# Optimization experiments

Measured on AMD Instinct MI355X. Metric: run time of the kernel, lower is better.

The kernel has to match this reference:

```python
import jax, jax.numpy as jnp
import numpy as np

D = 1024
H = 16
HD = D // H
EPS = 1e-5


def layer_norm(x, g, b):
    mu = jnp.mean(x, axis=-1, keepdims=True)
    var = jnp.var(x, axis=-1, keepdims=True)
    return (x - mu) * jax.lax.rsqrt(var + EPS) * g + b


def setup_inputs() -> dict:
    key = jax.random.key(0)
    ks = jax.random.split(key, 16)
    s = 0.02
    return {
        "x": jax.random.normal(ks[0], (2, 2048, D), jnp.float32),
        "ln1_g": jnp.ones((D,), jnp.float32),
        "ln1_b": jnp.zeros((D,), jnp.float32),
        "Wq": jax.random.normal(ks[1], (D, D), jnp.float32) * s,
        "bq": jnp.zeros((D,), jnp.float32),
        "Wk": jax.random.normal(ks[2], (D, D), jnp.float32) * s,
        "bk": jnp.zeros((D,), jnp.float32),
        "Wv": jax.random.normal(ks[3], (D, D), jnp.float32) * s,
        "bv": jnp.zeros((D,), jnp.float32),
        "Wo": jax.random.normal(ks[4], (D, D), jnp.float32) * s,
        "bo": jnp.zeros((D,), jnp.float32),
        "ln2_g": jnp.ones((D,), jnp.float32),
        "ln2_b": jnp.zeros((D,), jnp.float32),
        "W1": jax.random.normal(ks[5], (D, 4 * D), jnp.float32) * s,
        "b1": jnp.zeros((4 * D,), jnp.float32),
        "W2": jax.random.normal(ks[6], (4 * D, D), jnp.float32) * s,
        "b2": jnp.zeros((D,), jnp.float32),
    }


def reference(x, ln1_g, ln1_b, Wq, bq, Wk, bk, Wv, bv, Wo, bo, ln2_g, ln2_b, W1, b1, W2, b2):
    B, T, _ = x.shape
    # --- attention sub-block (pre-LN) ---
    h = layer_norm(x, ln1_g, ln1_b)
    q = (h @ Wq + bq).reshape(B, T, H, HD).transpose(0, 2, 1, 3)  # [B,H,T,hd]
    k = (h @ Wk + bk).reshape(B, T, H, HD).transpose(0, 2, 1, 3)
    v = (h @ Wv + bv).reshape(B, T, H, HD).transpose(0, 2, 1, 3)
    scores = jnp.einsum("bhqd,bhkd->bhqk", q, k)  # full O(T^2) scores as in source
    causal = jnp.tril(jnp.ones((T, T), bool))
    scores = jnp.where(causal, scores, -jnp.inf)
    w = jax.nn.softmax(scores / np.sqrt(HD), axis=-1)
    ctx = jnp.einsum("bhqk,bhkd->bhqd", w, v)
    ctx = ctx.transpose(0, 2, 1, 3).reshape(B, T, D)
    x = x + (ctx @ Wo + bo)
    # --- MLP sub-block (pre-LN) ---
    h = layer_norm(x, ln2_g, ln2_b)
    h = jax.nn.gelu(h @ W1 + b1, approximate=False)
    x = x + (h @ W2 + b2)
    return x
```

## Files before the change

kernel.cpp:

```cpp
#include <hip/hip_runtime.h>
#include <math.h>


typedef _Float16 half8 __attribute__((ext_vector_type(8)));
typedef _Float16 half4v __attribute__((ext_vector_type(4)));
typedef float floatx4 __attribute__((ext_vector_type(4)));

#define DMODEL 1024
#define SEQT   2048
#define NTOK   4096
#define NHEAD  16
#define HDIM   64

__device__ __forceinline__ void llds16(const _Float16* g, _Float16* l) {
  __builtin_amdgcn_global_load_lds(
      (const __attribute__((address_space(1))) void*)g,
      (__attribute__((address_space(3))) void*)l, 16, 0, 0);
}

__global__ __launch_bounds__(256) void wtrans_kernel(
    const float* __restrict__ Wq, const float* __restrict__ Wk,
    const float* __restrict__ Wv, const float* __restrict__ Wo,
    const float* __restrict__ W1, const float* __restrict__ W2,
    _Float16* __restrict__ wt_base) {
  __shared__ float tilebuf[32][33];
  int id = blockIdx.x;
  const float* src; _Float16* dst; int K, N, t;
  if (id < 4096) {
    int s = id >> 10;
    src = (s == 0) ? Wq : (s == 1) ? Wk : (s == 2) ? Wv : Wo;
    dst = wt_base + (size_t)s * (1024 * 1024);
    K = 1024; N = 1024; t = id & 1023;
  } else if (id < 8192) {
    src = W1; dst = wt_base + (size_t)4 * 1024 * 1024; K = 1024; N = 4096; t = id - 4096;
  } else {
    src = W2; dst = wt_base + (size_t)8 * 1024 * 1024; K = 4096; N = 1024; t = id - 8192;
  }
  int tilesN = N >> 5;
  int tk = t / tilesN, tn = t % tilesN;
  int c = threadIdx.x & 31, r0 = threadIdx.x >> 5;
#pragma unroll
  for (int i = 0; i < 4; ++i) {
    int r = r0 + i * 8;
    tilebuf[r][c] = src[(size_t)(tk * 32 + r) * N + tn * 32 + c];
  }
  __syncthreads();
#pragma unroll
  for (int i = 0; i < 4; ++i) {
    int r = r0 + i * 8;
    dst[(size_t)(tn * 32 + r) * K + tk * 32 + c] = (_Float16)tilebuf[c][r];
  }
}

__global__ __launch_bounds__(256) void ln_kernel(
    const float* __restrict__ x, const float* __restrict__ g,
    const float* __restrict__ b, _Float16* __restrict__ out) {
  int row = blockIdx.x;
  int t = threadIdx.x;
  const float4 xv = ((const float4*)(x + (size_t)row * DMODEL))[t];
  float s = xv.x + xv.y + xv.z + xv.w;
  float s2 = xv.x * xv.x + xv.y * xv.y + xv.z * xv.z + xv.w * xv.w;
#pragma unroll
  for (int off = 32; off; off >>= 1) {
    s += __shfl_down(s, off);
    s2 += __shfl_down(s2, off);
  }
  __shared__ float red[8];
  int wid = t >> 6;
  if ((t & 63) == 0) { red[wid] = s; red[wid + 4] = s2; }
  __syncthreads();
  s = red[0] + red[1] + red[2] + red[3];
  s2 = red[4] + red[5] + red[6] + red[7];
  float mu = s * (1.0f / DMODEL);
  float var = s2 * (1.0f / DMODEL) - mu * mu;
  float rstd = rsqrtf(var + 1e-5f);
  const float4 gv = ((const float4*)g)[t];
  const float4 bv = ((const float4*)b)[t];
  half4v o;
  o[0] = (_Float16)((xv.x - mu) * rstd * gv.x + bv.x);
  o[1] = (_Float16)((xv.y - mu) * rstd * gv.y + bv.y);
  o[2] = (_Float16)((xv.z - mu) * rstd * gv.z + bv.z);
  o[3] = (_Float16)((xv.w - mu) * rstd * gv.w + bv.w);
  *(half4v*)(out + (size_t)row * DMODEL + t * 4) = o;
}

template <int MODE>
__global__ __launch_bounds__(256) void gemm_kernel(
    const _Float16* __restrict__ A, const _Float16* __restrict__ Bt0, int K,
    const float* __restrict__ bias0, const float* __restrict__ bias1,
    const float* __restrict__ bias2, const float* __restrict__ res,
    float* __restrict__ outf, _Float16* __restrict__ outh) {
  constexpr int NT = (MODE == 1) ? 64 : 128;
  constexpr int MI = (NT == 128) ? 4 : 2;
  constexpr int BCH = NT / 64;
  __shared__ __align__(16) _Float16 As[2][128 * 32];
  __shared__ __align__(16) _Float16 Bs[2][NT * 32];
  const int tid = threadIdx.x;
  const int m0 = blockIdx.x * 128;
  const _Float16* Bt;
  const float* bias;
  _Float16* outh_sel = outh;
  int n0, sel = 0;
  if (MODE == 0) {
    sel = blockIdx.y >> 3;
    n0 = (blockIdx.y & 7) * 128;
    Bt = Bt0 + (size_t)sel * (1024 * 1024);
    bias = (sel == 0) ? bias0 : (sel == 1) ? bias1 : bias2;
    outh_sel = outh + (size_t)sel * ((size_t)NTOK * DMODEL);
  } else {
    n0 = blockIdx.y * NT;
    Bt = Bt0;
    bias = bias0;
  }
  const int w = tid >> 6, lane = tid & 63;
  const int l15 = lane & 15, q8 = lane >> 4;
  const int wrow = (NT == 128) ? (w >> 1) * 64 : w * 32;
  const int wcol = (NT == 128) ? (w & 1) * 64 : 0;

  const _Float16* gA[2]; int ldsA[2];
  const _Float16* gB[BCH]; int ldsB[BCH];
#pragma unroll
  for (int i = 0; i < 2; ++i) {
    int c0 = i * 256 + w * 64;
    int idx = c0 + lane;
    int m = idx >> 2, kq = (idx & 3) * 8;
    gA[i] = A + (size_t)(m0 + m) * K + kq;
    ldsA[i] = c0 * 8;
  }
#pragma unroll
  for (int i = 0; i < BCH; ++i) {
    int c0 = i * 256 + w * 64;
    int idx = c0 + lane;
    int m = idx >> 2, kq = (idx & 3) * 8;
    gB[i] = Bt + (size_t)(n0 + m) * K + kq;
    ldsB[i] = c0 * 8;
  }

  auto stage = [&](int buf) {
#pragma unroll
    for (int i = 0; i < 2; ++i) {
      llds16(gA[i], &As[buf][ldsA[i]]);
      gA[i] += 32;
    }
#pragma unroll
    for (int i = 0; i < BCH; ++i) {
      llds16(gB[i], &Bs[buf][ldsB[i]]);
      gB[i] += 32;
    }
  };

  floatx4 acc[MI][4];
#pragma unroll
  for (int i = 0; i < MI; ++i)
#pragma unroll
    for (int j = 0; j < 4; ++j) acc[i][j] = (floatx4){0.f, 0.f, 0.f, 0.f};

  const int nk = K >> 5;
  stage(0);
  __syncthreads();
  for (int t = 0; t < nk; ++t) {
    const int buf = t & 1;
    if (t + 1 < nk) stage(buf ^ 1);
    half8 af[MI], bf[4];
#pragma unroll
    for (int i = 0; i < MI; ++i)
      af[i] = *(const half8*)&As[buf][(wrow + i * 16 + l15) * 32 + q8 * 8];
#pragma unroll
    for (int j = 0; j < 4; ++j)
      bf[j] = *(const half8*)&Bs[buf][(wcol + j * 16 + l15) * 32 + q8 * 8];
#pragma unroll
    for (int i = 0; i < MI; ++i)
#pragma unroll
      for (int j = 0; j < 4; ++j)
        acc[i][j] = __builtin_amdgcn_mfma_f32_16x16x32_f16(af[i], bf[j], acc[i][j], 0, 0, 0);
    __syncthreads();
  }

#pragma unroll
  for (int i = 0; i < MI; ++i) {
    int rowb = m0 + wrow + i * 16 + q8 * 4;
#pragma unroll
    for (int j = 0; j < 4; ++j) {
      int col = n0 + wcol + j * 16 + l15;
      float bval = bias[col];
#pragma unroll
      for (int r = 0; r < 4; ++r) {
        int row = rowb + r;
        float v = acc[i][j][r] + bval;
        if (MODE == 0) {
          int bb = row >> 11, tt = row & 2047;
          int hh = col >> 6, hd = col & 63;
          if (sel == 2)
            outh_sel[((size_t)(bb * NHEAD + hh) * HDIM + hd) * SEQT + tt] = (_Float16)v;
          else
            outh_sel[((size_t)(bb * NHEAD + hh) * SEQT + tt) * HDIM + hd] = (_Float16)v;
        } else if (MODE == 1) {
          v += res[(size_t)row * 1024 + col];
          outf[(size_t)row * 1024 + col] = v;
        } else {
          float z = 1.5957691216f * v * (1.0f + 0.044715f * v * v);
          float gl = v / (1.0f + __expf(-z));
          outh[(size_t)row * 4096 + col] = (_Float16)gl;
        }
      }
    }
  }
}

__global__ __launch_bounds__(256) void attn_kernel(
    const _Float16* __restrict__ q, const _Float16* __restrict__ k,
    const _Float16* __restrict__ vt, _Float16* __restrict__ ctx) {
  __shared__ __align__(16) _Float16 Ks[2][64 * 64];
  __shared__ __align__(16) _Float16 Vs[2][64 * 64];
  __shared__ __align__(16) _Float16 Ps[64 * 72];
  __shared__ float Lpart[4][64];
  const int tid = threadIdx.x;
  const int w = tid >> 6, lane = tid & 63;
  const int l15 = lane & 15, q8 = lane >> 4;
  const int bh = blockIdx.y;
  const int pr = blockIdx.x;
  const size_t base = (size_t)bh * SEQT * HDIM;

  const _Float16* gk0[2]; const _Float16* gv0[2]; int ldsc[2];
#pragma unroll
  for (int i = 0; i < 2; ++i) {
    int c = i * 256 + w * 64 + lane;
    int r = c >> 3, gc = ((c & 7) ^ (r & 7)) * 8;
    gk0[i] = k + base + (size_t)r * HDIM + gc;
    gv0[i] = vt + base + (size_t)r * SEQT + gc;
    ldsc[i] = c * 8;
  }
  auto stage = [&](int kt, int buf) {
#pragma unroll
    for (int i = 0; i < 2; ++i) {
      llds16(gk0[i] + (size_t)kt * (64 * HDIM), &Ks[buf][ldsc[i]]);
      llds16(gv0[i] + kt * 64, &Vs[buf][ldsc[i]]);
    }
  };

  const int rswA = (l15 & 7);
  const int cs0 = (q8 ^ rswA) * 8;
  const int cs1 = ((4 + q8) ^ rswA) * 8;

  int s = 0;
  stage(0, 0);
  __syncthreads();
  for (int ph = 0; ph < 2; ++ph) {
    const int qtile = ph ? 31 - pr : pr;
    const int ntile = qtile + 1;
    half8 bq[4][2];
#pragma unroll
    for (int nt = 0; nt < 4; ++nt) {
      const half8* qp = (const half8*)(q + base + (size_t)(qtile * 64 + nt * 16 + l15) * HDIM);
      bq[nt][0] = qp[q8];
      bq[nt][1] = qp[4 + q8];
    }
    floatx4 acc[4];
#pragma unroll
    for (int j = 0; j < 4; ++j) acc[j] = (floatx4){0.f, 0.f, 0.f, 0.f};
    float lsum[4] = {0.f, 0.f, 0.f, 0.f};

    for (int jt = 0; jt < ntile; ++jt, ++s) {
      const int buf = s & 1;
      if (s + 1 < 33) {
        int sn = s + 1;
        int nkt = (sn <= pr) ? sn : sn - (pr + 1);
        stage(nkt, buf ^ 1);
      }
      half8 ak0 = *(const half8*)&Ks[buf][(w * 16 + l15) * 64 + cs0];
      half8 ak1 = *(const half8*)&Ks[buf][(w * 16 + l15) * 64 + cs1];
      floatx4 sv[4];
#pragma unroll
      for (int nt = 0; nt < 4; ++nt) {
        sv[nt] = __builtin_amdgcn_mfma_f32_16x16x32_f16(ak0, bq[nt][0],
                                                        (floatx4){0.f, 0.f, 0.f, 0.f}, 0, 0, 0);
        sv[nt] = __builtin_amdgcn_mfma_f32_16x16x32_f16(ak1, bq[nt][1], sv[nt], 0, 0, 0);
      }
      const bool diag = (jt == ntile - 1);
#pragma unroll
      for (int nt = 0; nt < 4; ++nt) {
        half4v phv;
#pragma unroll
        for (int r = 0; r < 4; ++r) {
          float p = __expf(sv[nt][r] * 0.125f);
          if (diag) {
            p = (w * 16 + q8 * 4 + r <= nt * 16 + l15) ? p : 0.f;
          }
          lsum[nt] += p;
          phv[r] = (_Float16)p;
        }
        *(half4v*)&Ps[(nt * 16 + l15) * 72 + w * 16 + q8 * 4] = phv;
      }
      __syncthreads();
      half8 ap0 = *(const half8*)&Ps[(w * 16 + l15) * 72 + q8 * 8];
      half8 ap1 = *(const half8*)&Ps[(w * 16 + l15) * 72 + 32 + q8 * 8];
#pragma unroll
      for (int ntd = 0; ntd < 4; ++ntd) {
        half8 bv0 = *(const half8*)&Vs[buf][(ntd * 16 + l15) * 64 + cs0];
        half8 bv1 = *(const half8*)&Vs[buf][(ntd * 16 + l15) * 64 + cs1];
        acc[ntd] = __builtin_amdgcn_mfma_f32_16x16x32_f16(ap0, bv0, acc[ntd], 0, 0, 0);
        acc[ntd] = __builtin_amdgcn_mfma_f32_16x16x32_f16(ap1, bv1, acc[ntd], 0, 0, 0);
      }
      __syncthreads();
    }

#pragma unroll
    for (int nt = 0; nt < 4; ++nt) {
      lsum[nt] += __shfl_xor(lsum[nt], 16);
      lsum[nt] += __shfl_xor(lsum[nt], 32);
      if (q8 == 0) Lpart[w][nt * 16 + l15] = lsum[nt];
    }
    __syncthreads();
    const int b = bh >> 4, h = bh & 15;
#pragma unroll
    for (int r = 0; r < 4; ++r) {
      int qr = w * 16 + q8 * 4 + r;
      float inv = 1.0f / (Lpart[0][qr] + Lpart[1][qr] + Lpart[2][qr] + Lpart[3][qr]);
      int tg = qtile * 64 + qr;
      _Float16* op = ctx + ((size_t)(b * SEQT + tg)) * DMODEL + h * HDIM;
#pragma unroll
      for (int ntd = 0; ntd < 4; ++ntd)
        op[ntd * 16 + l15] = (_Float16)(acc[ntd][r] * inv);
    }
  }
}

extern "C" void kernel_launch(void* const* d_in, const int* in_sizes, int n_in,
                              void* d_out, int out_size, void* d_ws, size_t ws_size,
                              hipStream_t stream) {
  (void)in_sizes; (void)n_in; (void)out_size; (void)ws_size;
  const float* x    = (const float*)d_in[0];
  const float* ln1g = (const float*)d_in[1];
  const float* ln1b = (const float*)d_in[2];
  const float* Wq   = (const float*)d_in[3];
  const float* bq   = (const float*)d_in[4];
  const float* Wk   = (const float*)d_in[5];
  const float* bk   = (const float*)d_in[6];
  const float* Wv   = (const float*)d_in[7];
  const float* bv   = (const float*)d_in[8];
  const float* Wo   = (const float*)d_in[9];
  const float* bo   = (const float*)d_in[10];
  const float* ln2g = (const float*)d_in[11];
  const float* ln2b = (const float*)d_in[12];
  const float* W1   = (const float*)d_in[13];
  const float* b1   = (const float*)d_in[14];
  const float* W2   = (const float*)d_in[15];
  const float* b2   = (const float*)d_in[16];
  float* out = (float*)d_out;

  char* ws = (char*)d_ws;
  _Float16* wt    = (_Float16*)(ws);
  _Float16* h16   = (_Float16*)(ws + ((size_t)24 << 20));
  _Float16* qkv   = (_Float16*)(ws + ((size_t)32 << 20));
  _Float16* ctx16 = (_Float16*)(ws + ((size_t)24 << 20));
  float*    x1    = (float*)   (ws + ((size_t)32 << 20));
  _Float16* h2    = (_Float16*)(ws + ((size_t)48 << 20));
  _Float16* mid   = (_Float16*)(ws + ((size_t)56 << 20));

  const size_t QKV1 = (size_t)NTOK * DMODEL;

  wtrans_kernel<<<12288, 256, 0, stream>>>(Wq, Wk, Wv, Wo, W1, W2, wt);
  ln_kernel<<<NTOK, 256, 0, stream>>>(x, ln1g, ln1b, h16);
  gemm_kernel<0><<<dim3(32, 24), 256, 0, stream>>>(
      h16, wt, 1024, bq, bk, bv, nullptr, nullptr, qkv);
  attn_kernel<<<dim3(16, 32), 256, 0, stream>>>(
      qkv, qkv + QKV1, qkv + 2 * QKV1, ctx16);
  gemm_kernel<1><<<dim3(32, 16), 256, 0, stream>>>(
      ctx16, wt + (size_t)3 * 1024 * 1024, 1024, bo, nullptr, nullptr, x, x1, nullptr);
  ln_kernel<<<NTOK, 256, 0, stream>>>(x1, ln2g, ln2b, h2);
  gemm_kernel<2><<<dim3(32, 32), 256, 0, stream>>>(
      h2, wt + (size_t)4 * 1024 * 1024, 1024, b1, nullptr, nullptr, nullptr, nullptr, mid);
  gemm_kernel<1><<<dim3(32, 16), 256, 0, stream>>>(
      mid, wt + (size_t)8 * 1024 * 1024, 4096, b2, nullptr, nullptr, x1, out, nullptr);
}
```

Before: 378.8 us.

## Use 128x128 tiles everywhere, XOR-swizzle LDS, split-K the W2 GEMM with atomics

The GEMM is unified to a 128x128 tile for all modes, so the out-projection now runs with 128-wide N tiles instead of 64. An XOR swizzle on the LDS column chunk is applied on both the global-to-LDS staging and the fragment reads, to reduce bank conflicts. The final K=4096 GEMM is split in two along K, with the output zeroed by a memset and both halves combined through float atomic adds; only the first half adds bias and residual. This raises block count for the W2 GEMM, which otherwise has only 256 blocks, at the cost of an extra memset, atomic traffic and non-deterministic summation order.

```diff
diff --git a/kernel.cpp b/kernel.cpp
--- a/kernel.cpp
+++ b/kernel.cpp
@@ -90,11 +90,8 @@
     const float* __restrict__ bias0, const float* __restrict__ bias1,
     const float* __restrict__ bias2, const float* __restrict__ res,
     float* __restrict__ outf, _Float16* __restrict__ outh) {
-  constexpr int NT = (MODE == 1) ? 64 : 128;
-  constexpr int MI = (NT == 128) ? 4 : 2;
-  constexpr int BCH = NT / 64;
   __shared__ __align__(16) _Float16 As[2][128 * 32];
-  __shared__ __align__(16) _Float16 Bs[2][NT * 32];
+  __shared__ __align__(16) _Float16 Bs[2][128 * 32];
   const int tid = threadIdx.x;
   const int m0 = blockIdx.x * 128;
   const _Float16* Bt;
@@ -108,68 +105,63 @@
     bias = (sel == 0) ? bias0 : (sel == 1) ? bias1 : bias2;
     outh_sel = outh + (size_t)sel * ((size_t)NTOK * DMODEL);
   } else {
-    n0 = blockIdx.y * NT;
+    n0 = blockIdx.y * 128;
     Bt = Bt0;
     bias = bias0;
   }
+  int Keff = K, koff = 0;
+  if (MODE == 3) { Keff = K >> 1; koff = blockIdx.z * Keff; }
   const int w = tid >> 6, lane = tid & 63;
   const int l15 = lane & 15, q8 = lane >> 4;
-  const int wrow = (NT == 128) ? (w >> 1) * 64 : w * 32;
-  const int wcol = (NT == 128) ? (w & 1) * 64 : 0;
-
-  const _Float16* gA[2]; int ldsA[2];
-  const _Float16* gB[BCH]; int ldsB[BCH];
+  const int wrow = (w >> 1) * 64;
+  const int wcol = (w & 1) * 64;
+  const int csw = (q8 ^ ((l15 >> 1) & 3)) * 8;
+
+  const _Float16* gA[2]; const _Float16* gB[2]; int ldsc[2];
 #pragma unroll
   for (int i = 0; i < 2; ++i) {
-    int c0 = i * 256 + w * 64;
-    int idx = c0 + lane;
-    int m = idx >> 2, kq = (idx & 3) * 8;
-    gA[i] = A + (size_t)(m0 + m) * K + kq;
-    ldsA[i] = c0 * 8;
-  }
-#pragma unroll
-  for (int i = 0; i < BCH; ++i) {
-    int c0 = i * 256 + w * 64;
-    int idx = c0 + lane;
-    int m = idx >> 2, kq = (idx & 3) * 8;
-    gB[i] = Bt + (size_t)(n0 + m) * K + kq;
-    ldsB[i] = c0 * 8;
+    int idx = i * 256 + w * 64 + lane;
+    int m = idx >> 2;
+    int kq = ((idx & 3) ^ ((m >> 1) & 3)) * 8;
+    gA[i] = A + (size_t)(m0 + m) * K + koff + kq;
+    gB[i] = Bt + (size_t)(n0 + m) * K + koff + kq;
+    ldsc[i] = idx * 8;
   }
 
   auto stage = [&](int buf) {
 #pragma unroll
     for (int i = 0; i < 2; ++i) {
-      llds16(gA[i], &As[buf][ldsA[i]]);
+      llds16(gA[i], &As[buf][ldsc[i]]);
       gA[i] += 32;
     }
 #pragma unroll
-    for (int i = 0; i < BCH; ++i) {
-      llds16(gB[i], &Bs[buf][ldsB[i]]);
+    for (int i = 0; i < 2; ++i) {
+      llds16(gB[i], &Bs[buf][ldsc[i]]);
       gB[i] += 32;
     }
   };
 
-  floatx4 acc[MI][4];
-#pragma unroll
-  for (int i = 0; i < MI; ++i)
+  floatx4 acc[4][4];
+#pragma unroll
+  for (int i = 0; i < 4; ++i)
 #pragma unroll
     for (int j = 0; j < 4; ++j) acc[i][j] = (floatx4){0.f, 0.f, 0.f, 0.f};
 
-  const int nk = K >> 5;
+  const int nk = Keff >> 5;
   stage(0);
   __syncthreads();
   for (int t = 0; t < nk; ++t) {
     const int buf = t & 1;
     if (t + 1 < nk) stage(buf ^ 1);
-    half8 af[MI], bf[4];
-#pragma unroll
-    for (int i = 0; i < MI; ++i)
-      af[i] = *(const half8*)&As[buf][(wrow + i * 16 + l15) * 32 + q8 * 8];
+    half8 af[4], bf[4];
+#pragma unroll
+    for (int i = 0; i < 4; ++i)
+      af[i] = *(const half8*)&As[buf][(wrow + i * 16 + l15) * 32 + csw];
 #pragma unroll
     for (int j = 0; j < 4; ++j)
-      bf[j] = *(const half8*)&Bs[buf][(wcol + j * 16 + l15) * 32 + q8 * 8];
-#pragma unroll
-    for (int i = 0; i < MI; ++i)
+      bf[j] = *(const half8*)&Bs[buf][(wcol + j * 16 + l15) * 32 + csw];
+#pragma unroll
+    for (int i = 0; i < 4; ++i)
 #pragma unroll
       for (int j = 0; j < 4; ++j)
         acc[i][j] = __builtin_amdgcn_mfma_f32_16x16x32_f16(af[i], bf[j], acc[i][j], 0, 0, 0);
@@ -177,7 +169,7 @@
   }
 
 #pragma unroll
-  for (int i = 0; i < MI; ++i) {
+  for (int i = 0; i < 4; ++i) {
     int rowb = m0 + wrow + i * 16 + q8 * 4;
 #pragma unroll
     for (int j = 0; j < 4; ++j) {
@@ -186,8 +178,9 @@
 #pragma unroll
       for (int r = 0; r < 4; ++r) {
         int row = rowb + r;
-        float v = acc[i][j][r] + bval;
+        float v = acc[i][j][r];
         if (MODE == 0) {
+          v += bval;
           int bb = row >> 11, tt = row & 2047;
           int hh = col >> 6, hd = col & 63;
           if (sel == 2)
@@ -195,12 +188,16 @@
           else
             outh_sel[((size_t)(bb * NHEAD + hh) * SEQT + tt) * HDIM + hd] = (_Float16)v;
         } else if (MODE == 1) {
-          v += res[(size_t)row * 1024 + col];
+          v += bval + res[(size_t)row * 1024 + col];
           outf[(size_t)row * 1024 + col] = v;
-        } else {
+        } else if (MODE == 2) {
+          v += bval;
           float z = 1.5957691216f * v * (1.0f + 0.044715f * v * v);
           float gl = v / (1.0f + __expf(-z));
           outh[(size_t)row * 4096 + col] = (_Float16)gl;
+        } else {
+          if (blockIdx.z == 0) v += bval + res[(size_t)row * 1024 + col];
+          unsafeAtomicAdd(outf + (size_t)row * 1024 + col, v);
         }
       }
     }
@@ -365,11 +362,12 @@
       h16, wt, 1024, bq, bk, bv, nullptr, nullptr, qkv);
   attn_kernel<<<dim3(16, 32), 256, 0, stream>>>(
       qkv, qkv + QKV1, qkv + 2 * QKV1, ctx16);
-  gemm_kernel<1><<<dim3(32, 16), 256, 0, stream>>>(
+  gemm_kernel<1><<<dim3(32, 8), 256, 0, stream>>>(
       ctx16, wt + (size_t)3 * 1024 * 1024, 1024, bo, nullptr, nullptr, x, x1, nullptr);
   ln_kernel<<<NTOK, 256, 0, stream>>>(x1, ln2g, ln2b, h2);
   gemm_kernel<2><<<dim3(32, 32), 256, 0, stream>>>(
       h2, wt + (size_t)4 * 1024 * 1024, 1024, b1, nullptr, nullptr, nullptr, nullptr, mid);
-  gemm_kernel<1><<<dim3(32, 16), 256, 0, stream>>>(
+  hipMemsetAsync(out, 0, (size_t)NTOK * DMODEL * sizeof(float), stream);
+  gemm_kernel<3><<<dim3(32, 8, 2), 256, 0, stream>>>(
       mid, wt + (size_t)8 * 1024 * 1024, 4096, b2, nullptr, nullptr, x1, out, nullptr);
 }
```

Result: no change. 382.0 us (+0.8%).
